# Kernel tuning notes

Hardware: AMD Instinct MI355X
Metric: run time of the kernel (lower is better)

The kernel has to match this reference:

```python
import jax, jax.numpy as jnp
import numpy as np

B, DIM = 8192, 64


def setup_inputs() -> dict:
    key = jax.random.key(0)
    m = jax.random.normal(key, (B, DIM, DIM), dtype=jnp.float32)
    # SPD input (covariance-like), positive trace so normA division is stable
    x = jnp.einsum('bij,bkj->bik', m, m) / DIM + 1e-3 * jnp.eye(DIM, dtype=jnp.float32)
    return {"x": x, "iterN": 5}


def reference(x, iterN):
    b, dim = x.shape[0], x.shape[1]
    I = jnp.eye(dim, dtype=x.dtype)  # [dim, dim]
    I3 = 3.0 * I                      # broadcast over batch
    # normA = (1/3) * sum(x * 3I) = trace(x)
    normA = jnp.trace(x, axis1=1, axis2=2)            # [B]
    A = x / normA[:, None, None]                       # [B, dim, dim]
    if iterN < 2:
        ZY = 0.5 * (I3 - A)
        YZY = jnp.matmul(A, ZY)
    else:
        ZY = 0.5 * (I3 - A)
        Y = jnp.matmul(A, ZY)
        Z = ZY
        for _ in range(1, iterN - 1):
            ZY = 0.5 * (I3 - jnp.matmul(Z, Y))
            Y = jnp.matmul(Y, ZY)
            Z = jnp.matmul(ZY, Z)
        YZY = 0.5 * jnp.matmul(Y, I3 - jnp.matmul(Z, Y))
    y = YZY * jnp.sqrt(normA)[:, None, None]
    return y
```

## Files before the change

### kernel.cpp

```cpp
#include <hip/hip_runtime.h>

#define DIM 64
#define LSTRIDE 68
#define PLANE (DIM * LSTRIDE)

typedef __attribute__((ext_vector_type(8))) short short8;
typedef __attribute__((ext_vector_type(16))) float f32x16;

#define MFMA(a, b, c) __builtin_amdgcn_mfma_f32_32x32x16_bf16((a), (b), (c), 0, 0, 0)

__device__ __forceinline__ void split_hl(float v, unsigned int& uh, unsigned int& ul) {
    unsigned int u = __float_as_uint(v);
    uh = (u + 0x8000u) & 0xffff0000u;
    float lo = v - __uint_as_float(uh);
    ul = __float_as_uint(lo);
}

union FragU { short8 v; uint2 u2[2]; };

__device__ __forceinline__ short8 load_frag(const unsigned short* p) {
    FragU f;
    f.u2[0] = *(const uint2*)p;
    f.u2[1] = *(const uint2*)(p + 4);
    return f.v;
}

extern "C" __global__ void __launch_bounds__(256, 3)
isqrtm_kernel(const float* __restrict__ x, const int* __restrict__ iterN_p,
              float* __restrict__ out)
{
    __shared__ __align__(16) unsigned short pl[6][PLANE];
    __shared__ float s_tr;

    const int t = threadIdx.x;
    const int b = blockIdx.x;
    const float* xg = x + (size_t)b * 4096;
    float* og = out + (size_t)b * 4096;
    const int iterN = iterN_p[0];

    if (t < 64) {
        float v = xg[t * 65];
        #pragma unroll
        for (int o = 32; o > 0; o >>= 1) v += __shfl_down(v, o);
        if (t == 0) s_tr = v;
    }
    __syncthreads();
    const float tr  = s_tr;
    const float inv = 1.0f / tr;
    const float sc  = sqrtf(tr);

    #pragma unroll
    for (int ch = 0; ch < 4; ++ch) {
        const int e  = ch * 1024 + t * 4;
        const int i  = e >> 6, j0 = e & 63;
        const float4 xv = *(const float4*)(xg + e);
        const float av[4] = { xv.x * inv, xv.y * inv, xv.z * inv, xv.w * inv };
        unsigned int ahu[4], alu[4], zhu[4], zlu[4];
        #pragma unroll
        for (int q = 0; q < 4; ++q) {
            split_hl(av[q], ahu[q], alu[q]);
            const float z = fmaf(-0.5f, av[q], (i == j0 + q) ? 1.5f : 0.0f);
            split_hl(z, zhu[q], zlu[q]);
        }
        const int ad = i * LSTRIDE + j0;
        *(uint2*)&pl[0][ad] = make_uint2((ahu[0] >> 16) | ahu[1], (ahu[2] >> 16) | ahu[3]);
        *(uint2*)&pl[1][ad] = make_uint2((alu[0] >> 16) | (alu[1] & 0xffff0000u),
                                         (alu[2] >> 16) | (alu[3] & 0xffff0000u));
        *(uint2*)&pl[4][ad] = make_uint2((zhu[0] >> 16) | zhu[1], (zhu[2] >> 16) | zhu[3]);
        *(uint2*)&pl[5][ad] = make_uint2((zlu[0] >> 16) | (zlu[1] & 0xffff0000u),
                                         (zlu[2] >> 16) | (zlu[3] & 0xffff0000u));
    }
    __syncthreads();

    const int lane = t & 63;
    const int wv = t >> 6;
    const int wr = wv >> 1, wc = wv & 1;
    const int m  = lane & 31, hh = lane >> 5;
    const int ra = (32 * wr + m) * LSTRIDE + 8 * hh;
    const int rb = (32 * wc + m) * LSTRIDE + 8 * hh;
    const int dql = 32 * wc + m - 32 * wr - 4 * hh;

    short8 yh[4], yl[4];

    auto load_B = [&](int p_) {
        #pragma unroll
        for (int s = 0; s < 4; ++s) {
            yh[s] = load_frag(&pl[p_][rb + 16 * s]);
            yl[s] = load_frag(&pl[p_ + 1][rb + 16 * s]);
        }
    };

    auto matmul_cB = [&](int a_) -> f32x16 {
        f32x16 acc = {};
        #pragma unroll
        for (int s = 0; s < 4; ++s) {
            const short8 ah = load_frag(&pl[a_][ra + 16 * s]);
            const short8 al = load_frag(&pl[a_ + 1][ra + 16 * s]);
            acc = MFMA(ah, yh[s], acc);
            acc = MFMA(ah, yl[s], acc);
            acc = MFMA(al, yh[s], acc);
        }
        return acc;
    };

    auto matmul2_cB = [&](int b2_, f32x16& o1, f32x16& o2) {
        o1 = {}; o2 = {};
        #pragma unroll
        for (int s = 0; s < 4; ++s) {
            const short8 ah  = load_frag(&pl[0][ra + 16 * s]);
            const short8 al  = load_frag(&pl[1][ra + 16 * s]);
            const short8 b2h = load_frag(&pl[b2_][rb + 16 * s]);
            const short8 b2l = load_frag(&pl[b2_ + 1][rb + 16 * s]);
            o1 = MFMA(ah, yh[s], o1); o1 = MFMA(ah, yl[s], o1); o1 = MFMA(al, yh[s], o1);
            o2 = MFMA(ah, b2h, o2);   o2 = MFMA(ah, b2l, o2);   o2 = MFMA(al, b2h, o2);
        }
    };

    auto write_tile = [&](int p_, const f32x16& acc, bool zyform) {
        #pragma unroll
        for (int g = 0; g < 4; ++g) {
            unsigned int uh[4], ul[4];
            #pragma unroll
            for (int q = 0; q < 4; ++q) {
                float v = acc[4 * g + q];
                if (zyform)
                    v = fmaf(-0.5f, v, (q + 8 * g == dql) ? 1.5f : 0.0f);
                split_hl(v, uh[q], ul[q]);
            }
            const int ad = (32 * wc + m) * LSTRIDE + (32 * wr + 8 * g + 4 * hh);
            *(uint2*)&pl[p_][ad]     = make_uint2((uh[0] >> 16) | uh[1], (uh[2] >> 16) | uh[3]);
            *(uint2*)&pl[p_ + 1][ad] = make_uint2((ul[0] >> 16) | (ul[1] & 0xffff0000u),
                                                  (ul[2] >> 16) | (ul[3] & 0xffff0000u));
        }
    };

    auto write_global = [&](const f32x16& acc, float scale) {
        #pragma unroll
        for (int g = 0; g < 4; ++g)
            #pragma unroll
            for (int q = 0; q < 4; ++q) {
                const int rl = q + 8 * g + 4 * hh;
                og[(32 * wr + rl) * 64 + 32 * wc + m] = acc[4 * g + q] * scale;
            }
    };

    {
        load_B(4);
        const f32x16 accY = matmul_cB(0);
        if (iterN < 2) { write_global(accY, sc); return; }
        write_tile(2, accY, false);
    }
    __syncthreads();

    for (int it = 1; it < iterN - 1; ++it) {
        load_B(2);
        const f32x16 T = matmul_cB(4);
        write_tile(0, T, true);
        __syncthreads();
        f32x16 nY, nZ;
        matmul2_cB(4, nY, nZ);
        __syncthreads();
        write_tile(2, nY, false);
        write_tile(4, nZ, false);
        __syncthreads();
    }

    {
        load_B(2);
        const f32x16 T = matmul_cB(4);
        write_tile(0, T, true);
        __syncthreads();
        const f32x16 O = matmul_cB(0);
        write_global(O, sc);
    }
}

extern "C" void kernel_launch(void* const* d_in, const int* in_sizes, int n_in,
                              void* d_out, int out_size, void* d_ws, size_t ws_size,
                              hipStream_t stream) {
    const float* x = (const float*)d_in[0];
    const int* iterN = (const int*)d_in[1];
    float* out = (float*)d_out;
    const int B = in_sizes[0] / (DIM * DIM);
    isqrtm_kernel<<<dim3(B), dim3(256), 0, stream>>>(x, iterN, out);
}
```

Before: 321.8 us.

## Interleave hi/lo bf16 planes in LDS, use packed bf16 convert, vectorize output stores

Merges the separate hi and lo bf16 planes into one dword-strided buffer per matrix, with the hi and lo halves 32 dwords apart in each row, and changes the row padding. Splitting now uses the hardware packed bf16 convert when the builtin exists, with a round-to-nearest-even fallback otherwise. The global write is changed to float4 stores by exploiting symmetry (transposed indexing). This is meant to cut ALU work in the splits, shift LDS bank patterns and coalesce the output writes. In exchange, the transposed write relies on the result being symmetric, and the new stride may cause different bank conflicts.

```diff
diff --git a/kernel.cpp b/kernel.cpp
--- a/kernel.cpp
+++ b/kernel.cpp
@@ -1,35 +1,56 @@
 #include <hip/hip_runtime.h>
 
 #define DIM 64
-#define LSTRIDE 68
-#define PLANE (DIM * LSTRIDE)
+#define RSTRIDE 66
+#define BUFDW (DIM * RSTRIDE)
 
 typedef __attribute__((ext_vector_type(8))) short short8;
 typedef __attribute__((ext_vector_type(16))) float f32x16;
+#if __has_builtin(__builtin_amdgcn_cvt_pk_bf16_f32)
+typedef __attribute__((ext_vector_type(2))) __bf16 bf16x2;
+#endif
 
 #define MFMA(a, b, c) __builtin_amdgcn_mfma_f32_32x32x16_bf16((a), (b), (c), 0, 0, 0)
 
-__device__ __forceinline__ void split_hl(float v, unsigned int& uh, unsigned int& ul) {
-    unsigned int u = __float_as_uint(v);
-    uh = (u + 0x8000u) & 0xffff0000u;
-    float lo = v - __uint_as_float(uh);
-    ul = __float_as_uint(lo);
+__device__ __forceinline__ void split_pk(float v0, float v1,
+                                         unsigned int& hp, unsigned int& lp) {
+#if __has_builtin(__builtin_amdgcn_cvt_pk_bf16_f32)
+    bf16x2 h = __builtin_amdgcn_cvt_pk_bf16_f32(v0, v1);
+    hp = __builtin_bit_cast(unsigned int, h);
+    const float h0 = __uint_as_float(hp << 16);
+    const float h1 = __uint_as_float(hp & 0xffff0000u);
+    bf16x2 l = __builtin_amdgcn_cvt_pk_bf16_f32(v0 - h0, v1 - h1);
+    lp = __builtin_bit_cast(unsigned int, l);
+#else
+    unsigned int u0 = __float_as_uint(v0), u1 = __float_as_uint(v1);
+    unsigned int r0 = (u0 + 0x7fffu + ((u0 >> 16) & 1u)) & 0xffff0000u;
+    unsigned int r1 = (u1 + 0x7fffu + ((u1 >> 16) & 1u)) & 0xffff0000u;
+    hp = (r0 >> 16) | r1;
+    float l0 = v0 - __uint_as_float(r0), l1 = v1 - __uint_as_float(r1);
+    unsigned int w0 = __float_as_uint(l0), w1 = __float_as_uint(l1);
+    unsigned int s0 = (w0 + 0x7fffu + ((w0 >> 16) & 1u)) & 0xffff0000u;
+    unsigned int s1 = (w1 + 0x7fffu + ((w1 >> 16) & 1u)) & 0xffff0000u;
+    lp = (s0 >> 16) | s1;
+#endif
 }
 
 union FragU { short8 v; uint2 u2[2]; };
 
-__device__ __forceinline__ short8 load_frag(const unsigned short* p) {
-    FragU f;
-    f.u2[0] = *(const uint2*)p;
-    f.u2[1] = *(const uint2*)(p + 4);
-    return f.v;
+__device__ __forceinline__ void load_frag_hl(const unsigned int* bp, int off,
+                                             short8& h, short8& l) {
+    FragU fh, fl;
+    fh.u2[0] = *(const uint2*)(bp + off);
+    fl.u2[0] = *(const uint2*)(bp + off + 32);
+    fh.u2[1] = *(const uint2*)(bp + off + 2);
+    fl.u2[1] = *(const uint2*)(bp + off + 34);
+    h = fh.v; l = fl.v;
 }
 
 extern "C" __global__ void __launch_bounds__(256, 3)
 isqrtm_kernel(const float* __restrict__ x, const int* __restrict__ iterN_p,
               float* __restrict__ out)
 {
-    __shared__ __align__(16) unsigned short pl[6][PLANE];
+    __shared__ __align__(16) unsigned int bufs[3][BUFDW];
     __shared__ float s_tr;
 
     const int t = threadIdx.x;
@@ -54,21 +75,21 @@
         const int e  = ch * 1024 + t * 4;
         const int i  = e >> 6, j0 = e & 63;
         const float4 xv = *(const float4*)(xg + e);
-        const float av[4] = { xv.x * inv, xv.y * inv, xv.z * inv, xv.w * inv };
-        unsigned int ahu[4], alu[4], zhu[4], zlu[4];
-        #pragma unroll
-        for (int q = 0; q < 4; ++q) {
-            split_hl(av[q], ahu[q], alu[q]);
-            const float z = fmaf(-0.5f, av[q], (i == j0 + q) ? 1.5f : 0.0f);
-            split_hl(z, zhu[q], zlu[q]);
-        }
-        const int ad = i * LSTRIDE + j0;
-        *(uint2*)&pl[0][ad] = make_uint2((ahu[0] >> 16) | ahu[1], (ahu[2] >> 16) | ahu[3]);
-        *(uint2*)&pl[1][ad] = make_uint2((alu[0] >> 16) | (alu[1] & 0xffff0000u),
-                                         (alu[2] >> 16) | (alu[3] & 0xffff0000u));
-        *(uint2*)&pl[4][ad] = make_uint2((zhu[0] >> 16) | zhu[1], (zhu[2] >> 16) | zhu[3]);
-        *(uint2*)&pl[5][ad] = make_uint2((zlu[0] >> 16) | (zlu[1] & 0xffff0000u),
-                                         (zlu[2] >> 16) | (zlu[3] & 0xffff0000u));
+        const float a0 = xv.x * inv, a1 = xv.y * inv, a2 = xv.z * inv, a3 = xv.w * inv;
+        unsigned int ah0, al0, ah1, al1, zh0, zl0, zh1, zl1;
+        split_pk(a0, a1, ah0, al0);
+        split_pk(a2, a3, ah1, al1);
+        const float z0 = fmaf(-0.5f, a0, (i == j0)     ? 1.5f : 0.0f);
+        const float z1 = fmaf(-0.5f, a1, (i == j0 + 1) ? 1.5f : 0.0f);
+        const float z2 = fmaf(-0.5f, a2, (i == j0 + 2) ? 1.5f : 0.0f);
+        const float z3 = fmaf(-0.5f, a3, (i == j0 + 3) ? 1.5f : 0.0f);
+        split_pk(z0, z1, zh0, zl0);
+        split_pk(z2, z3, zh1, zl1);
+        const int ad = i * RSTRIDE + (j0 >> 1);
+        *(uint2*)&bufs[0][ad]      = make_uint2(ah0, ah1);
+        *(uint2*)&bufs[0][ad + 32] = make_uint2(al0, al1);
+        *(uint2*)&bufs[2][ad]      = make_uint2(zh0, zh1);
+        *(uint2*)&bufs[2][ad + 32] = make_uint2(zl0, zl1);
     }
     __syncthreads();
 
@@ -76,26 +97,25 @@
     const int wv = t >> 6;
     const int wr = wv >> 1, wc = wv & 1;
     const int m  = lane & 31, hh = lane >> 5;
-    const int ra = (32 * wr + m) * LSTRIDE + 8 * hh;
-    const int rb = (32 * wc + m) * LSTRIDE + 8 * hh;
+    const int ra0 = (32 * wr + m) * RSTRIDE + 4 * hh;
+    const int rb0 = (32 * wc + m) * RSTRIDE + 4 * hh;
+    const int wb0 = (32 * wc + m) * RSTRIDE + 16 * wr + 2 * hh;
     const int dql = 32 * wc + m - 32 * wr - 4 * hh;
 
     short8 yh[4], yl[4];
 
-    auto load_B = [&](int p_) {
+    auto load_B = [&](const unsigned int* bp) {
+        #pragma unroll
+        for (int s = 0; s < 4; ++s)
+            load_frag_hl(bp, rb0 + 8 * s, yh[s], yl[s]);
+    };
+
+    auto matmul_cB = [&](const unsigned int* ap) -> f32x16 {
+        f32x16 acc = {};
         #pragma unroll
         for (int s = 0; s < 4; ++s) {
-            yh[s] = load_frag(&pl[p_][rb + 16 * s]);
-            yl[s] = load_frag(&pl[p_ + 1][rb + 16 * s]);
-        }
-    };
-
-    auto matmul_cB = [&](int a_) -> f32x16 {
-        f32x16 acc = {};
-        #pragma unroll
-        for (int s = 0; s < 4; ++s) {
-            const short8 ah = load_frag(&pl[a_][ra + 16 * s]);
-            const short8 al = load_frag(&pl[a_ + 1][ra + 16 * s]);
+            short8 ah, al;
+            load_frag_hl(ap, ra0 + 8 * s, ah, al);
             acc = MFMA(ah, yh[s], acc);
             acc = MFMA(ah, yl[s], acc);
             acc = MFMA(al, yh[s], acc);
@@ -103,74 +123,75 @@
         return acc;
     };
 
-    auto matmul2_cB = [&](int b2_, f32x16& o1, f32x16& o2) {
+    auto matmul2_cB = [&](const unsigned int* ap, const unsigned int* b2p,
+                          f32x16& o1, f32x16& o2) {
         o1 = {}; o2 = {};
         #pragma unroll
         for (int s = 0; s < 4; ++s) {
-            const short8 ah  = load_frag(&pl[0][ra + 16 * s]);
-            const short8 al  = load_frag(&pl[1][ra + 16 * s]);
-            const short8 b2h = load_frag(&pl[b2_][rb + 16 * s]);
-            const short8 b2l = load_frag(&pl[b2_ + 1][rb + 16 * s]);
+            short8 ah, al, b2h, b2l;
+            load_frag_hl(ap,  ra0 + 8 * s, ah,  al);
+            load_frag_hl(b2p, rb0 + 8 * s, b2h, b2l);
             o1 = MFMA(ah, yh[s], o1); o1 = MFMA(ah, yl[s], o1); o1 = MFMA(al, yh[s], o1);
             o2 = MFMA(ah, b2h, o2);   o2 = MFMA(ah, b2l, o2);   o2 = MFMA(al, b2h, o2);
         }
     };
 
-    auto write_tile = [&](int p_, const f32x16& acc, bool zyform) {
+    auto write_tile = [&](unsigned int* bp, const f32x16& acc, bool zyform) {
         #pragma unroll
         for (int g = 0; g < 4; ++g) {
-            unsigned int uh[4], ul[4];
+            float v[4];
             #pragma unroll
             for (int q = 0; q < 4; ++q) {
-                float v = acc[4 * g + q];
+                v[q] = acc[4 * g + q];
                 if (zyform)
-                    v = fmaf(-0.5f, v, (q + 8 * g == dql) ? 1.5f : 0.0f);
-                split_hl(v, uh[q], ul[q]);
+                    v[q] = fmaf(-0.5f, v[q], (q + 8 * g == dql) ? 1.5f : 0.0f);
             }
-            const int ad = (32 * wc + m) * LSTRIDE + (32 * wr + 8 * g + 4 * hh);
-            *(uint2*)&pl[p_][ad]     = make_uint2((uh[0] >> 16) | uh[1], (uh[2] >> 16) | uh[3]);
-            *(uint2*)&pl[p_ + 1][ad] = make_uint2((ul[0] >> 16) | (ul[1] & 0xffff0000u),
-                                                  (ul[2] >> 16) | (ul[3] & 0xffff0000u));
+            unsigned int h01, l01, h23, l23;
+            split_pk(v[0], v[1], h01, l01);
+            split_pk(v[2], v[3], h23, l23);
+            const int ad = wb0 + 4 * g;
+            *(uint2*)&bp[ad]      = make_uint2(h01, h23);
+            *(uint2*)&bp[ad + 32] = make_uint2(l01, l23);
         }
     };
 
     auto write_global = [&](const f32x16& acc, float scale) {
-        #pragma unroll
-        for (int g = 0; g < 4; ++g)
-            #pragma unroll
-            for (int q = 0; q < 4; ++q) {
-                const int rl = q + 8 * g + 4 * hh;
-                og[(32 * wr + rl) * 64 + 32 * wc + m] = acc[4 * g + q] * scale;
-            }
+        float* rowp = og + (32 * wc + m) * 64 + 32 * wr + 4 * hh;
+        #pragma unroll
+        for (int g = 0; g < 4; ++g) {
+            float4 o4 = make_float4(acc[4 * g] * scale, acc[4 * g + 1] * scale,
+                                    acc[4 * g + 2] * scale, acc[4 * g + 3] * scale);
+            *(float4*)(rowp + 8 * g) = o4;
+        }
     };
 
     {
-        load_B(4);
-        const f32x16 accY = matmul_cB(0);
+        load_B(bufs[2]);
+        const f32x16 accY = matmul_cB(bufs[0]);
         if (iterN < 2) { write_global(accY, sc); return; }
-        write_tile(2, accY, false);
+        write_tile(bufs[1], accY, false);
     }
     __syncthreads();
 
     for (int it = 1; it < iterN - 1; ++it) {
-        load_B(2);
-        const f32x16 T = matmul_cB(4);
-        write_tile(0, T, true);
+        load_B(bufs[1]);
+        const f32x16 T = matmul_cB(bufs[2]);
+        write_tile(bufs[0], T, true);
         __syncthreads();
         f32x16 nY, nZ;
-        matmul2_cB(4, nY, nZ);
-        __syncthreads();
-        write_tile(2, nY, false);
-        write_tile(4, nZ, false);
+        matmul2_cB(bufs[0], bufs[2], nY, nZ);
+        __syncthreads();
+        write_tile(bufs[1], nY, false);
+        write_tile(bufs[2], nZ, false);
         __syncthreads();
     }
 
     {
-        load_B(2);
-        const f32x16 T = matmul_cB(4);
-        write_tile(0, T, true);
-        __syncthreads();
-        const f32x16 O = matmul_cB(0);
+        load_B(bufs[1]);
+        const f32x16 T = matmul_cB(bufs[2]);
+        write_tile(bufs[0], T, true);
+        __syncthreads();
+        const f32x16 O = matmul_cB(bufs[0]);
         write_global(O, sc);
     }
 }
```

After: 346.7 us. 1.08x slower.
